# Optimization experiments

Measured on AMD Instinct MI355X. Metric: run time of the kernel, lower is better.

Reference implementation:

```python
import jax, jax.numpy as jnp
import numpy as np

INPUT_SIZE = 500
SENTENCE_SIZE = 128


def setup_inputs() -> dict:
    key = jax.random.key(0)
    ks = jax.random.split(key, 20)
    B, D = 16, 512
    Ho, Hi, Hu = 4, 4, 4
    dh_ori = D // Ho          # 128
    dh = D // (Hi + Hu)       # 64
    s = 0.05
    code = jax.random.normal(ks[0], (B, INPUT_SIZE, D), jnp.float32)
    # binary sentence-membership mask (which code tokens belong to each sentence)
    input_sentence = (jax.random.uniform(ks[1], (B, SENTENCE_SIZE, INPUT_SIZE)) < 0.2).astype(jnp.float32)

    def W(k, h, dout):
        return jax.random.normal(k, (h, D, dout), jnp.float32) * s

    def b(k, h, dout):
        return jax.random.normal(k, (h, dout), jnp.float32) * 0.01

    return dict(
        code=code, input_sentence=input_sentence,
        Wq_ori=W(ks[2], Ho, dh_ori), bq_ori=b(ks[3], Ho, dh_ori),
        Wk_ori=W(ks[4], Ho, dh_ori), bk_ori=b(ks[5], Ho, dh_ori),
        Wq_in=W(ks[6], Hi, dh), bq_in=b(ks[7], Hi, dh),
        Wk_in=W(ks[8], Hi, dh), bk_in=b(ks[9], Hi, dh),
        Wv_in=W(ks[10], Hi, dh), bv_in=b(ks[11], Hi, dh),
        Wq_out=W(ks[12], Hu, dh), bq_out=b(ks[13], Hu, dh),
        Wk_out=W(ks[14], Hu, dh), bk_out=b(ks[15], Hu, dh),
        Wv_out=W(ks[16], Hu, dh), bv_out=b(ks[17], Hu, dh),
    )


def _proj(x, W, b):
    # x: (B, N, D), W: (H, D, F), b: (H, F) -> (B, H, N, F), relu Dense per head
    return jax.nn.relu(jnp.einsum('bnd,hdf->bhnf', x, W) + b[:, None, :])


def reference(code, input_sentence,
              Wq_ori, bq_ori, Wk_ori, bk_ori,
              Wq_in, bq_in, Wk_in, bk_in, Wv_in, bv_in,
              Wq_out, bq_out, Wk_out, bk_out, Wv_out, bv_out):
    B, S = input_sentence.shape[0], input_sentence.shape[1]
    sent = input_sentence

    # ---- original (ori) branch: max over heads of raw QK^T, mask, matmul code ----
    q = _proj(code, Wq_ori, bq_ori)
    k = _proj(code, Wk_ori, bk_ori)
    scores_ori = jnp.einsum('bhnf,bhmf->bhnm', q, k).max(axis=1)      # (B, N, N)
    sA = jnp.einsum('bsn,bnm->bsm', sent, scores_ori)                 # (B, S, N)
    out_ori = jnp.einsum('bsm,bmd->bsd', sent * sA, code)             # (B, S, D)

    # ---- in-mask heads ----
    qi = _proj(code, Wq_in, bq_in)
    ki = _proj(code, Wk_in, bk_in)
    vi = _proj(code, Wv_in, bv_in)
    sc = jnp.einsum('bhnf,bhmf->bhnm', qi, ki)                        # (B, Hi, N, N)
    sAi = jnp.einsum('bsn,bhnm->bhsm', sent, sc)                      # (B, Hi, S, N)
    out_in = jnp.einsum('bhsm,bhmf->bhsf', sent[:, None] * sAi, vi)   # (B, Hi, S, F)

    # ---- out-mask heads ----
    qo = _proj(code, Wq_out, bq_out)
    ko = _proj(code, Wk_out, bk_out)
    vo = _proj(code, Wv_out, bv_out)
    sco = jnp.einsum('bhnf,bhmf->bhnm', qo, ko)
    sAo = jnp.einsum('bsn,bhnm->bhsm', sent, sco)
    masked = (sent - 1.0)[:, None] * sAo                              # (B, Hu, S, N)
    include = sent.sum(axis=2)[:, None, :, None]                      # (B, 1, S, 1)
    masked = masked / (INPUT_SIZE - include) * include
    out_out = jnp.einsum('bhsm,bhmf->bhsf', masked, vo)               # (B, Hu, S, F)

    # original returns a list [ori, in_0..in_Hi-1, out_0..out_Hu-1]; concat along features
    in_flat = jnp.transpose(out_in, (0, 2, 1, 3)).reshape(B, S, -1)
    out_flat = jnp.transpose(out_out, (0, 2, 1, 3)).reshape(B, S, -1)
    return jnp.concatenate([out_ori, in_flat, out_flat], axis=-1)
```

## Files before the change

kernel.cpp:

```cpp
#include <hip/hip_runtime.h>
#include <cfloat>

#define B_  16
#define N_  500
#define NP  512
#define S_  128
#define D_  512
#define FO  128
#define FI  64

typedef unsigned short u16;
typedef __attribute__((ext_vector_type(8))) short bf8;
typedef __attribute__((ext_vector_type(4))) float f4;

#define MFMA(a,b,c) __builtin_amdgcn_mfma_f32_16x16x32_bf16((a),(b),(c),0,0,0)

__device__ __forceinline__ u16 f2b(float x){
    union{float f;unsigned u;} v; v.f=x;
    unsigned r = v.u + 0x7fffu + ((v.u>>16)&1u);
    return (u16)(r>>16);
}
__device__ __forceinline__ float b2f(u16 x){
    union{unsigned u;float f;} v; v.u=((unsigned)x)<<16; return v.f;
}
__device__ __forceinline__ bf8 ldb8(const u16* p){ return *(const bf8*)p; }

__device__ __forceinline__ void gl2lds16(const u16* g, u16* lds){
    __builtin_amdgcn_global_load_lds(
        (const __attribute__((address_space(1))) unsigned int*)g,
        (__attribute__((address_space(3))) unsigned int*)lds, 16, 0, 0);
}

__global__ __launch_bounds__(256) void prep_code(const float* __restrict__ code,
                                                 u16* __restrict__ codeB,
                                                 u16* __restrict__ codeT)
{
    __shared__ float T[64][65];
    const int b = blockIdx.x, m0 = blockIdx.y*64, d0 = blockIdx.z*64;
    const int t = threadIdx.x;
    #pragma unroll
    for (int i=0;i<16;++i){
        int idx = t + i*256; int rr = idx>>6, cc = idx&63;
        int m = m0+rr;
        T[rr][cc] = (m < N_) ? code[((size_t)b*N_+m)*D_ + d0+cc] : 0.f;
    }
    __syncthreads();
    #pragma unroll
    for (int i=0;i<16;++i){
        int idx=t+i*256; int rr=idx>>6, cc=idx&63; int m=m0+rr;
        if (m<N_) codeB[((size_t)b*N_+m)*D_ + d0+cc] = f2b(T[rr][cc]);
    }
    #pragma unroll
    for (int i=0;i<16;++i){
        int idx=t+i*256; int dd=idx>>6, mm=idx&63;
        codeT[((size_t)b*D_ + d0+dd)*NP + m0+mm] = f2b(T[mm][dd]);
    }
}

__global__ __launch_bounds__(128) void prep_sent(const float* __restrict__ sent,
                                                 u16* __restrict__ sentB,
                                                 float* __restrict__ inc)
{
    const int b=blockIdx.x, s=blockIdx.y, t=threadIdx.x;
    const float* row = sent + ((size_t)b*S_+s)*N_;
    float4 v = make_float4(0.f,0.f,0.f,0.f);
    const int n = t*4;
    if (n < N_) v = *(const float4*)(row+n);
    float sum = v.x+v.y+v.z+v.w;
    ushort4 o; o.x=f2b(v.x); o.y=f2b(v.y); o.z=f2b(v.z); o.w=f2b(v.w);
    *(ushort4*)&sentB[((size_t)b*S_+s)*NP + n] = o;
    #pragma unroll
    for (int off=32; off; off>>=1) sum += __shfl_down(sum, off);
    __shared__ float ls[2];
    if ((t&63)==0) ls[t>>6]=sum;
    __syncthreads();
    if (t==0) inc[b*S_+s] = ls[0]+ls[1];
}

struct PWAll { const float* W[8]; u16* WT[8]; };
__global__ __launch_bounds__(256) void prep_w_all(PWAll a)
{
    const int slot = blockIdx.y;
    const int widx = slot<4 ? (slot>>1) : slot-2;
    const int ftile= slot<4 ? (slot&1)  : 0;
    const int F    = slot<4 ? 128 : 64;
    const float* W = a.W[widx];
    u16* WT        = a.WT[widx];
    __shared__ float T[64][65];
    const int h=blockIdx.x, f0=ftile*64, d0=blockIdx.z*64, t=threadIdx.x;
    #pragma unroll
    for (int i=0;i<16;++i){
        int idx=t+i*256; int rr=idx>>6, cc=idx&63;
        T[rr][cc] = W[((size_t)h*D_ + d0+rr)*F + f0+cc];
    }
    __syncthreads();
    #pragma unroll
    for (int i=0;i<16;++i){
        int idx=t+i*256; int ff=idx>>6, dd=idx&63;
        WT[((size_t)h*F + f0+ff)*D_ + d0+dd] = f2b(T[dd][ff]);
    }
}

__global__ __launch_bounds__(256) void zero_pad4(u16* a0, u16* a1, u16* a2, u16* a3)
{
    u16* arr4[4] = {a0,a1,a2,a3};
    u16* base = arr4[blockIdx.y] + (size_t)blockIdx.x*FI*NP;
    for (int idx=threadIdx.x; idx<FI*12; idx+=256){
        int f = idx/12, n = N_ + idx%12;
        base[(size_t)f*NP + n] = 0;
    }
}

struct GemmOut { const float* bias[8]; u16* dst[8]; };
__global__ __launch_bounds__(256) void proj_gemm(const u16* __restrict__ codeB,
                                                 const u16* __restrict__ WallT,
                                                 GemmOut go)
{
    __shared__ alignas(16) u16 As[2][128*32];
    __shared__ alignas(16) u16 Bs[2][128*32];
    const int t = threadIdx.x;
    const int w = t>>6, l = t&63, lane16 = l&15, lq = l>>4;
    const int r0 = blockIdx.x*128;
    const int c0 = blockIdx.y*128;
    const int wr = (w>>1)*64, wc = (w&1)*64;
    const int srow = l>>2;
    const int scol = (l&3)*8;

    f4 acc[4][4] = {};

    auto STAGE = [&](int buf, int k0){
        #pragma unroll
        for (int iss=0; iss<2; ++iss){
            const int rbase = w*32 + iss*16;
            gl2lds16(codeB + (size_t)(r0+rbase+srow)*D_ + k0 + scol, &As[buf][rbase*32]);
            gl2lds16(WallT + (size_t)(c0+rbase+srow)*D_ + k0 + scol, &Bs[buf][rbase*32]);
        }
    };

    STAGE(0, 0);
    int buf = 0;
    for (int k0=0; k0<D_; k0+=32){
        __syncthreads();
        if (k0+32 < D_) STAGE(buf^1, k0+32);
        bf8 af[4], bfr[4];
        #pragma unroll
        for (int i=0;i<4;++i){
            af[i]  = *(const bf8*)&As[buf][(wr + i*16 + lane16)*32 + lq*8];
            bfr[i] = *(const bf8*)&Bs[buf][(wc + i*16 + lane16)*32 + lq*8];
        }
        #pragma unroll
        for (int i=0;i<4;++i)
            #pragma unroll
            for (int j=0;j<4;++j)
                acc[i][j] = MFMA(af[i], bfr[j], acc[i][j]);
        buf ^= 1;
    }
    #pragma unroll
    for (int j=0;j<4;++j){
        const int c = c0 + wc + j*16 + lane16;
        int ri, hf, F;
        if (c < 1024){ ri = c>>9; hf = c & 511; F = 128; }
        else { const int u = c-1024; ri = 2 + (u>>8); hf = u & 255; F = 64; }
        const float bv = go.bias[ri][hf];
        const int h  = (F==128) ? (hf>>7) : (hf>>6);
        const int f2 = hf & (F-1);
        const bool tr = (ri>=2) && (ri!=3) && (ri!=6);
        #pragma unroll
        for (int i=0;i<4;++i){
            const int rb = r0 + wr + i*16 + lq*4;
            if (rb >= 8000) continue;
            const int b  = rb / 500;
            const int n0 = rb % 500;
            float v[4];
            #pragma unroll
            for (int reg=0;reg<4;++reg){
                float x = acc[i][j][reg] + bv;
                v[reg] = x>0.f ? x : 0.f;
            }
            if (tr){
                ushort4 o4; o4.x=f2b(v[0]); o4.y=f2b(v[1]); o4.z=f2b(v[2]); o4.w=f2b(v[3]);
                *(ushort4*)&go.dst[ri][((size_t)(b*4+h)*FI + f2)*NP + n0] = o4;
            } else {
                u16* o = go.dst[ri] + ((size_t)(b*4+h)*N_ + n0)*F + f2;
                #pragma unroll
                for (int reg=0;reg<4;++reg) o[(size_t)reg*F] = f2b(v[reg]);
            }
        }
    }
}

__global__ __launch_bounds__(256) void ms_mfma(const u16* __restrict__ q,
                                               const u16* __restrict__ k,
                                               u16* __restrict__ maxscT)
{
    __shared__ alignas(16) u16 Qs[64][136];
    __shared__ alignas(16) u16 Ks[128][136];
    const int t=threadIdx.x, w=t>>6, l=t&63, lane16=l&15, lq=l>>4;
    const int b=blockIdx.x, n0=blockIdx.y*64, m0=blockIdx.z*128;
    const int wr=(w>>1)*32, wc=(w&1)*64;

    f4 best[2][4];
    #pragma unroll
    for(int rt=0;rt<2;++rt)
        #pragma unroll
        for(int ct=0;ct<4;++ct)
            #pragma unroll
            for(int i=0;i<4;++i) best[rt][ct][i] = -FLT_MAX;

    for (int h=0;h<4;++h){
        const u16* qh = q + (size_t)(b*4+h)*N_*FO;
        const u16* kh = k + (size_t)(b*4+h)*N_*FO;
        #pragma unroll
        for (int i=0;i<4;++i){
            const int e=t+i*256, row=e>>4, kc=(e&15)*8;
            int n=n0+row; if(n>N_-1)n=N_-1;
            *(bf8*)&Qs[row][kc] = ldb8(qh + (size_t)n*FO + kc);
        }
        #pragma unroll
        for (int i=0;i<8;++i){
            const int e=t+i*256, row=e>>4, kc=(e&15)*8;
            int m=m0+row; if(m>N_-1)m=N_-1;
            *(bf8*)&Ks[row][kc] = ldb8(kh + (size_t)m*FO + kc);
        }
        __syncthreads();
        f4 acc[2][4]={};
        #pragma unroll
        for (int kk=0;kk<FO;kk+=32){
            bf8 a0=*(const bf8*)&Qs[wr+lane16][kk+lq*8];
            bf8 a1=*(const bf8*)&Qs[wr+16+lane16][kk+lq*8];
            #pragma unroll
            for(int ct=0;ct<4;++ct){
                bf8 bb=*(const bf8*)&Ks[wc+ct*16+lane16][kk+lq*8];
                acc[0][ct]=MFMA(a0,bb,acc[0][ct]);
                acc[1][ct]=MFMA(a1,bb,acc[1][ct]);
            }
        }
        #pragma unroll
        for(int rt=0;rt<2;++rt)
            #pragma unroll
            for(int ct=0;ct<4;++ct)
                #pragma unroll
                for(int i=0;i<4;++i) best[rt][ct][i] = fmaxf(best[rt][ct][i], acc[rt][ct][i]);
        __syncthreads();
    }
    #pragma unroll
    for(int rt=0;rt<2;++rt)
        #pragma unroll
        for(int ct=0;ct<4;++ct){
            const int m  = m0+wc+ct*16+lane16;
            const int nb = n0+wr+rt*16+lq*4;
            if (m < N_ && nb < N_){
                ushort4 o; o.x=f2b(best[rt][ct][0]); o.y=f2b(best[rt][ct][1]);
                o.z=f2b(best[rt][ct][2]); o.w=f2b(best[rt][ct][3]);
                *(ushort4*)&maxscT[((size_t)b*NP+m)*NP + nb] = o;
            }
        }
}

__global__ __launch_bounds__(512) void saoo(const u16* __restrict__ sentB,
                                            const u16* __restrict__ maxscT,
                                            const u16* __restrict__ codeT,
                                            float* __restrict__ out)
{
    __shared__ u16 sAmS[16][520];
    const int b=blockIdx.x, s0=blockIdx.y*16;
    const int t=threadIdx.x, w=t>>6, l=t&63, lane16=l&15, lq=l>>4;

    {
        const int m0 = w*64;
        const u16* ap = sentB + ((size_t)b*S_ + s0+lane16)*NP + lq*8;
        const u16* bp[4];
        #pragma unroll
        for(int ct=0;ct<4;++ct) bp[ct] = maxscT + ((size_t)b*NP + m0+ct*16+lane16)*NP + lq*8;
        f4 acc[4] = {};
        for (int k0=0;k0<NP;k0+=32){
            bf8 av=ldb8(ap+k0);
            #pragma unroll
            for(int ct=0;ct<4;++ct) acc[ct]=MFMA(av, ldb8(bp[ct]+k0), acc[ct]);
        }
        #pragma unroll
        for(int ct=0;ct<4;++ct){
            const int m = m0+ct*16+lane16;
            #pragma unroll
            for(int reg=0;reg<4;++reg){
                const int s = s0+lq*4+reg;
                const float sv = b2f(sentB[((size_t)b*S_+s)*NP+m]);
                sAmS[lq*4+reg][m] = f2b(acc[ct][reg]*sv);
            }
        }
    }
    __syncthreads();
    {
        const int d0 = w*64;
        const u16* bp[4];
        #pragma unroll
        for(int ct=0;ct<4;++ct) bp[ct] = codeT + ((size_t)b*D_ + d0+ct*16+lane16)*NP + lq*8;
        f4 acc[4] = {};
        for (int k0=0;k0<NP;k0+=32){
            bf8 av = *(const bf8*)&sAmS[lane16][k0+lq*8];
            #pragma unroll
            for(int ct=0;ct<4;++ct) acc[ct]=MFMA(av, ldb8(bp[ct]+k0), acc[ct]);
        }
        #pragma unroll
        for(int ct=0;ct<4;++ct){
            const int d = d0+ct*16+lane16;
            #pragma unroll
            for(int reg=0;reg<4;++reg){
                const int s = s0+lq*4+reg;
                out[((size_t)b*S_+s)*1024 + d] = acc[ct][reg];
            }
        }
    }
}

struct AttnArgs { const u16* qT[2]; const u16* kp[2]; const u16* vT[2]; };
__global__ __launch_bounds__(256) void attn_fused(AttnArgs a,
                                                  const u16* __restrict__ sentB,
                                                  const float* __restrict__ inc,
                                                  float* __restrict__ out)
{
    __shared__ float red[4][32][68];
    __shared__ u16 qsS[32][72];
    __shared__ u16 Pw[4][32][72];
    const int bh=blockIdx.x, b=bh>>2, h=bh&3, s0=blockIdx.y*32, br=blockIdx.z;
    const u16* qT = a.qT[br];
    const u16* kp = a.kp[br];
    const u16* vT = a.vT[br];
    const int t=threadIdx.x, w=t>>6, l=t&63, lane16=l&15, lq=l>>4;

    {
        const u16 *ap[2], *bp[4];
        #pragma unroll
        for(int rt=0;rt<2;++rt) ap[rt] = sentB + ((size_t)b*S_ + s0+rt*16+lane16)*NP + w*128 + lq*8;
        #pragma unroll
        for(int ct=0;ct<4;++ct) bp[ct] = qT + ((size_t)bh*FI + ct*16+lane16)*NP + w*128 + lq*8;
        f4 acc[2][4] = {};
        #pragma unroll
        for (int k0=0;k0<128;k0+=32){
            bf8 a0=ldb8(ap[0]+k0), a1=ldb8(ap[1]+k0);
            #pragma unroll
            for(int ct=0;ct<4;++ct){
                bf8 bb=ldb8(bp[ct]+k0);
                acc[0][ct]=MFMA(a0,bb,acc[0][ct]);
                acc[1][ct]=MFMA(a1,bb,acc[1][ct]);
            }
        }
        #pragma unroll
        for(int rt=0;rt<2;++rt)
            #pragma unroll
            for(int ct=0;ct<4;++ct)
                #pragma unroll
                for(int reg=0;reg<4;++reg)
                    red[w][rt*16+lq*4+reg][ct*16+lane16] = acc[rt][ct][reg];
    }
    __syncthreads();
    {
        const int s=t>>3, f0=(t&7)*8;
        #pragma unroll
        for (int j=0;j<8;++j){
            float v = red[0][s][f0+j]+red[1][s][f0+j]+red[2][s][f0+j]+red[3][s][f0+j];
            qsS[s][f0+j] = f2b(v);
        }
    }
    __syncthreads();

    f4 accO[2][4] = {};
    #pragma unroll
    for (int c=0;c<2;++c){
        const int m0 = w*64 + c*256;
        f4 p[2][4] = {};
        const u16* bp[4];
        #pragma unroll
        for(int ct=0;ct<4;++ct){
            int m=m0+ct*16+lane16; if(m>N_-1)m=N_-1;
            bp[ct] = kp + ((size_t)bh*N_+m)*FI + lq*8;
        }
        #pragma unroll
        for (int kk=0; kk<FI; kk+=32){
            bf8 a0 = *(const bf8*)&qsS[lane16][kk+lq*8];
            bf8 a1 = *(const bf8*)&qsS[16+lane16][kk+lq*8];
            #pragma unroll
            for(int ct=0;ct<4;++ct){
                bf8 bb=ldb8(bp[ct]+kk);
                p[0][ct]=MFMA(a0,bb,p[0][ct]);
                p[1][ct]=MFMA(a1,bb,p[1][ct]);
            }
        }
        #pragma unroll
        for(int rt=0;rt<2;++rt)
            #pragma unroll
            for(int ct=0;ct<4;++ct){
                const int m = m0+ct*16+lane16;
                #pragma unroll
                for(int reg=0;reg<4;++reg){
                    const int s = s0+rt*16+lq*4+reg;
                    const float sv = b2f(sentB[((size_t)b*S_+s)*NP+m]);
                    const float wgt = br ? ((m<N_)? sv-1.f : 0.f) : sv;
                    Pw[w][rt*16+lq*4+reg][ct*16+lane16] = f2b(p[rt][ct][reg]*wgt);
                }
            }
        #pragma unroll
        for (int kk2=0; kk2<64; kk2+=32){
            bf8 a2[2];
            #pragma unroll
            for(int rt=0;rt<2;++rt) a2[rt] = *(const bf8*)&Pw[w][rt*16+lane16][kk2+lq*8];
            #pragma unroll
            for(int ct=0;ct<4;++ct){
                bf8 vv = ldb8(vT + ((size_t)bh*FI + ct*16+lane16)*NP + m0+kk2+lq*8);
                accO[0][ct]=MFMA(a2[0],vv,accO[0][ct]);
                accO[1][ct]=MFMA(a2[1],vv,accO[1][ct]);
            }
        }
    }
    #pragma unroll
    for(int rt=0;rt<2;++rt)
        #pragma unroll
        for(int ct=0;ct<4;++ct)
            #pragma unroll
            for(int reg=0;reg<4;++reg)
                red[w][rt*16+lq*4+reg][ct*16+lane16] = accO[rt][ct][reg];
    __syncthreads();
    {
        const int s=t>>3, f0=(t&7)*8;
        float fac = 1.f;
        if (br){ const float ic = inc[b*S_+s0+s]; fac = ic/(500.f-ic); }
        const size_t o = ((size_t)b*S_+s0+s)*1024 + (br?768:512) + h*FI + f0;
        #pragma unroll
        for (int j=0;j<8;++j){
            float v = red[0][s][f0+j]+red[1][s][f0+j]+red[2][s][f0+j]+red[3][s][f0+j];
            out[o+j] = v*fac;
        }
    }
}

extern "C" void kernel_launch(void* const* d_in, const int* in_sizes, int n_in,
                              void* d_out, int out_size, void* d_ws, size_t ws_size,
                              hipStream_t stream)
{
    const float* code   = (const float*)d_in[0];
    const float* sent   = (const float*)d_in[1];
    const float* Wq_ori = (const float*)d_in[2];
    const float* bq_ori = (const float*)d_in[3];
    const float* Wk_ori = (const float*)d_in[4];
    const float* bk_ori = (const float*)d_in[5];
    const float* Wq_in  = (const float*)d_in[6];
    const float* bq_in  = (const float*)d_in[7];
    const float* Wk_in  = (const float*)d_in[8];
    const float* bk_in  = (const float*)d_in[9];
    const float* Wv_in  = (const float*)d_in[10];
    const float* bv_in  = (const float*)d_in[11];
    const float* Wq_out = (const float*)d_in[12];
    const float* bq_out = (const float*)d_in[13];
    const float* Wk_out = (const float*)d_in[14];
    const float* bk_out = (const float*)d_in[15];
    const float* Wv_out = (const float*)d_in[16];
    const float* bv_out = (const float*)d_in[17];
    float* out = (float*)d_out;

    char* w = (char*)d_ws;
    u16*   codeB  = (u16*)(w);
    u16*   WallT  = (u16*)(w + 8257536);
    u16*   WTqo   = WallT;
    u16*   WTko   = WallT +  262144;
    u16*   WTqi   = WallT +  524288;
    u16*   WTki   = WallT +  655360;
    u16*   WTvi   = WallT +  786432;
    u16*   WTqu   = WallT +  917504;
    u16*   WTku   = WallT + 1048576;
    u16*   WTvu   = WallT + 1179648;
    u16*   sentB  = (u16*)(w + 10878976);
    float* incp   = (float*)(w + 12976128);
    u16* q_ori  = (u16*)(w + 12984320);
    u16* k_ori  = (u16*)(w + 21176320);
    u16* maxscT = (u16*)(w + 29368320);
    u16* codeT  = (u16*)(w + 37756928);
    u16* k_in   = (u16*)(w + 46145536);
    u16* k_out  = (u16*)(w + 50241536);
    u16* qT_in  = (u16*)(w + 54337536);
    u16* qT_out = (u16*)(w + 58531840);
    u16* vT_in  = (u16*)(w + 62726144);
    u16* vT_out = (u16*)(w + 66920448);

    prep_code<<<dim3(16,8,8), 256, 0, stream>>>(code, codeB, codeT);
    prep_sent<<<dim3(16,128), 128, 0, stream>>>(sent, sentB, incp);
    PWAll pw;
    pw.W[0]=Wq_ori; pw.W[1]=Wk_ori; pw.W[2]=Wq_in; pw.W[3]=Wk_in;
    pw.W[4]=Wv_in;  pw.W[5]=Wq_out; pw.W[6]=Wk_out; pw.W[7]=Wv_out;
    pw.WT[0]=WTqo; pw.WT[1]=WTko; pw.WT[2]=WTqi; pw.WT[3]=WTki;
    pw.WT[4]=WTvi; pw.WT[5]=WTqu; pw.WT[6]=WTku; pw.WT[7]=WTvu;
    prep_w_all<<<dim3(4,10,8), 256, 0, stream>>>(pw);
    zero_pad4<<<dim3(64,4), 256, 0, stream>>>(qT_in, qT_out, vT_in, vT_out);

    GemmOut go;
    go.bias[0]=bq_ori; go.bias[1]=bk_ori; go.bias[2]=bq_in; go.bias[3]=bk_in;
    go.bias[4]=bv_in;  go.bias[5]=bq_out; go.bias[6]=bk_out; go.bias[7]=bv_out;
    go.dst[0]=q_ori; go.dst[1]=k_ori; go.dst[2]=qT_in; go.dst[3]=k_in;
    go.dst[4]=vT_in; go.dst[5]=qT_out; go.dst[6]=k_out; go.dst[7]=vT_out;
    proj_gemm<<<dim3(63,20), 256, 0, stream>>>(codeB, WallT, go);

    ms_mfma<<<dim3(16,8,4), 256, 0, stream>>>(q_ori, k_ori, maxscT);
    saoo<<<dim3(16,8), 512, 0, stream>>>(sentB, maxscT, codeT, out);

    AttnArgs aa;
    aa.qT[0]=qT_in;  aa.qT[1]=qT_out;
    aa.kp[0]=k_in;   aa.kp[1]=k_out;
    aa.vT[0]=vT_in;  aa.vT[1]=vT_out;
    attn_fused<<<dim3(64,4,2), 256, 0, stream>>>(aa, sentB, incp, out);
}
```

Baseline: 136.9 us.

## Stage proj_gemm epilogue through LDS for coalesced stores and remap blocks per XCD

The projection GEMM epilogue now writes biased, ReLU'd bf16 tiles into a shared-memory buffer that aliases the operand staging area, then streams them out as coalesced ushort4 rows in either the transposed or the natural layout. The launch changes to a 1D grid of 1280 blocks with an XCD-aware mapping, so blocks sharing row tiles of codeB land on the same XCD for L2 reuse. The K loop is unrolled by two with explicit vmcnt drains, and the workspace grows so 64 row tiles (8192 rows) of codeB fit. Smaller edits remove bounds checks in ms_mfma stores and skip the multiply when the sentence mask is zero. These add an extra LDS round trip and barrier, and the unguarded ms_mfma stores rely on padding being writable.

```diff
diff --git a/kernel.cpp b/kernel.cpp
--- a/kernel.cpp
+++ b/kernel.cpp
@@ -29,6 +29,9 @@
     __builtin_amdgcn_global_load_lds(
         (const __attribute__((address_space(1))) unsigned int*)g,
         (__attribute__((address_space(3))) unsigned int*)lds, 16, 0, 0);
+}
+__device__ __forceinline__ void vdrain(){
+    asm volatile("s_waitcnt vmcnt(0)" ::: "memory");
 }
 
 __global__ __launch_bounds__(256) void prep_code(const float* __restrict__ code,
@@ -112,79 +115,126 @@
 }
 
 struct GemmOut { const float* bias[8]; u16* dst[8]; };
+union ProjLDS {
+    u16 ab[4][4096];
+    u16 ot[16896];
+};
 __global__ __launch_bounds__(256) void proj_gemm(const u16* __restrict__ codeB,
                                                  const u16* __restrict__ WallT,
                                                  GemmOut go)
 {
-    __shared__ alignas(16) u16 As[2][128*32];
-    __shared__ alignas(16) u16 Bs[2][128*32];
+    __shared__ alignas(16) ProjLDS L;
+
     const int t = threadIdx.x;
     const int w = t>>6, l = t&63, lane16 = l&15, lq = l>>4;
-    const int r0 = blockIdx.x*128;
-    const int c0 = blockIdx.y*128;
+    const int bid = blockIdx.x;
+    const int xcd = bid & 7;
+    const int g   = bid >> 3;
+    const int rt  = xcd*8 + g/20;
+    const int ct  = g - (g/20)*20;
+    const int r0 = rt*128;
+    const int c0 = ct*128;
     const int wr = (w>>1)*64, wc = (w&1)*64;
     const int srow = l>>2;
     const int scol = (l&3)*8;
 
     f4 acc[4][4] = {};
 
-    auto STAGE = [&](int buf, int k0){
+    auto STAGE = [&](u16* Ad, u16* Bd, int k0){
         #pragma unroll
         for (int iss=0; iss<2; ++iss){
             const int rbase = w*32 + iss*16;
-            gl2lds16(codeB + (size_t)(r0+rbase+srow)*D_ + k0 + scol, &As[buf][rbase*32]);
-            gl2lds16(WallT + (size_t)(c0+rbase+srow)*D_ + k0 + scol, &Bs[buf][rbase*32]);
+            gl2lds16(codeB + (size_t)(r0+rbase+srow)*D_ + k0 + scol, Ad + rbase*32);
+            gl2lds16(WallT + (size_t)(c0+rbase+srow)*D_ + k0 + scol, Bd + rbase*32);
         }
     };
-
-    STAGE(0, 0);
-    int buf = 0;
-    for (int k0=0; k0<D_; k0+=32){
-        __syncthreads();
-        if (k0+32 < D_) STAGE(buf^1, k0+32);
+    auto COMPUTE = [&](const u16* Ad, const u16* Bd){
         bf8 af[4], bfr[4];
         #pragma unroll
         for (int i=0;i<4;++i){
-            af[i]  = *(const bf8*)&As[buf][(wr + i*16 + lane16)*32 + lq*8];
-            bfr[i] = *(const bf8*)&Bs[buf][(wc + i*16 + lane16)*32 + lq*8];
+            af[i]  = *(const bf8*)&Ad[(wr + i*16 + lane16)*32 + lq*8];
+            bfr[i] = *(const bf8*)&Bd[(wc + i*16 + lane16)*32 + lq*8];
         }
         #pragma unroll
         for (int i=0;i<4;++i)
             #pragma unroll
             for (int j=0;j<4;++j)
                 acc[i][j] = MFMA(af[i], bfr[j], acc[i][j]);
-        buf ^= 1;
-    }
+    };
+
+    STAGE(L.ab[0], L.ab[2], 0);
+    #pragma unroll
+    for (int k0=0; k0<D_; k0+=64){
+        vdrain(); __syncthreads();
+        if (k0+32 < D_) STAGE(L.ab[1], L.ab[3], k0+32);
+        COMPUTE(L.ab[0], L.ab[2]);
+        vdrain(); __syncthreads();
+        if (k0+64 < D_) STAGE(L.ab[0], L.ab[2], k0+64);
+        COMPUTE(L.ab[1], L.ab[3]);
+    }
+
+    const int ri = (ct<4) ? 0 : (ct<8) ? 1 : 2 + ((ct-8)>>1);
+    const bool tr = (ri==2)||(ri==4)||(ri==5)||(ri==7);
+
+    vdrain(); __syncthreads();
+
     #pragma unroll
     for (int j=0;j<4;++j){
         const int c = c0 + wc + j*16 + lane16;
-        int ri, hf, F;
-        if (c < 1024){ ri = c>>9; hf = c & 511; F = 128; }
-        else { const int u = c-1024; ri = 2 + (u>>8); hf = u & 255; F = 64; }
-        const float bv = go.bias[ri][hf];
-        const int h  = (F==128) ? (hf>>7) : (hf>>6);
-        const int f2 = hf & (F-1);
-        const bool tr = (ri>=2) && (ri!=3) && (ri!=6);
-        #pragma unroll
-        for (int i=0;i<4;++i){
-            const int rb = r0 + wr + i*16 + lq*4;
-            if (rb >= 8000) continue;
-            const int b  = rb / 500;
-            const int n0 = rb % 500;
-            float v[4];
-            #pragma unroll
-            for (int reg=0;reg<4;++reg){
-                float x = acc[i][j][reg] + bv;
-                v[reg] = x>0.f ? x : 0.f;
-            }
-            if (tr){
-                ushort4 o4; o4.x=f2b(v[0]); o4.y=f2b(v[1]); o4.z=f2b(v[2]); o4.w=f2b(v[3]);
-                *(ushort4*)&go.dst[ri][((size_t)(b*4+h)*FI + f2)*NP + n0] = o4;
-            } else {
-                u16* o = go.dst[ri] + ((size_t)(b*4+h)*N_ + n0)*F + f2;
+        const int idx = (c < 1024) ? (c & 511) : ((c-1024) & 255);
+        const float bv = go.bias[ri][idx];
+        if (tr){
+            #pragma unroll
+            for (int i=0;i<4;++i){
+                ushort4 o4;
+                float x0=acc[i][j][0]+bv, x1=acc[i][j][1]+bv, x2=acc[i][j][2]+bv, x3=acc[i][j][3]+bv;
+                o4.x=f2b(x0>0.f?x0:0.f); o4.y=f2b(x1>0.f?x1:0.f);
+                o4.z=f2b(x2>0.f?x2:0.f); o4.w=f2b(x3>0.f?x3:0.f);
+                *(ushort4*)&L.ot[(wc+j*16+lane16)*132 + wr+i*16+lq*4] = o4;
+            }
+        } else {
+            #pragma unroll
+            for (int i=0;i<4;++i)
                 #pragma unroll
-                for (int reg=0;reg<4;++reg) o[(size_t)reg*F] = f2b(v[reg]);
-            }
+                for (int reg=0;reg<4;++reg){
+                    float x = acc[i][j][reg] + bv;
+                    L.ot[(wr+i*16+lq*4+reg)*132 + wc+j*16+lane16] = f2b(x>0.f?x:0.f);
+                }
+        }
+    }
+    __syncthreads();
+
+    if (tr){
+        const int c  = t>>1;
+        const int cg = c0 + c;
+        const int u  = cg - 1024;
+        const int hfv = u & 255, h = hfv>>6, f2 = hfv & 63;
+        u16* dbase = go.dst[ri];
+        const int half = t & 1;
+        #pragma unroll
+        for (int k2=0;k2<16;++k2){
+            const int r  = half*64 + k2*4;
+            const int rb = r0 + r;
+            if (rb < 8000){
+                const int b = rb/500, n = rb - b*500;
+                *(ushort4*)&dbase[((size_t)(b*4+h)*FI + f2)*NP + n] =
+                    *(const ushort4*)&L.ot[c*132 + r];
+            }
+        }
+    } else {
+        const int r  = t>>1;
+        const int rb = r0 + r;
+        if (rb < 8000){
+            const int b = rb/500, n = rb - b*500;
+            const int half = t & 1;
+            const int cg0 = c0 + half*64;
+            int h, f2base, F2;
+            if (cg0 < 1024){ const int hf0 = cg0 & 511; h = hf0>>7; f2base = hf0 & 127; F2 = 128; }
+            else           { const int hf0 = (cg0-1024) & 255; h = hf0>>6; f2base = hf0 & 63; F2 = 64; }
+            u16* dstp = go.dst[ri] + ((size_t)(b*4+h)*N_ + n)*F2 + f2base;
+            #pragma unroll
+            for (int k2=0;k2<16;++k2)
+                *(ushort4*)&dstp[k2*4] = *(const ushort4*)&L.ot[r*132 + half*64 + k2*4];
         }
     }
 }
@@ -249,11 +299,9 @@
         for(int ct=0;ct<4;++ct){
             const int m  = m0+wc+ct*16+lane16;
             const int nb = n0+wr+rt*16+lq*4;
-            if (m < N_ && nb < N_){
-                ushort4 o; o.x=f2b(best[rt][ct][0]); o.y=f2b(best[rt][ct][1]);
-                o.z=f2b(best[rt][ct][2]); o.w=f2b(best[rt][ct][3]);
-                *(ushort4*)&maxscT[((size_t)b*NP+m)*NP + nb] = o;
-            }
+            ushort4 o; o.x=f2b(best[rt][ct][0]); o.y=f2b(best[rt][ct][1]);
+            o.z=f2b(best[rt][ct][2]); o.w=f2b(best[rt][ct][3]);
+            *(ushort4*)&maxscT[((size_t)b*NP+m)*NP + nb] = o;
         }
 }
 
@@ -285,7 +333,7 @@
             for(int reg=0;reg<4;++reg){
                 const int s = s0+lq*4+reg;
                 const float sv = b2f(sentB[((size_t)b*S_+s)*NP+m]);
-                sAmS[lq*4+reg][m] = f2b(acc[ct][reg]*sv);
+                sAmS[lq*4+reg][m] = (sv != 0.f) ? f2b(acc[ct][reg]*sv) : (u16)0;
             }
         }
     }
@@ -459,7 +507,7 @@
 
     char* w = (char*)d_ws;
     u16*   codeB  = (u16*)(w);
-    u16*   WallT  = (u16*)(w + 8257536);
+    u16*   WallT  = (u16*)(w + 8388608);
     u16*   WTqo   = WallT;
     u16*   WTko   = WallT +  262144;
     u16*   WTqi   = WallT +  524288;
@@ -468,18 +516,18 @@
     u16*   WTqu   = WallT +  917504;
     u16*   WTku   = WallT + 1048576;
     u16*   WTvu   = WallT + 1179648;
-    u16*   sentB  = (u16*)(w + 10878976);
-    float* incp   = (float*)(w + 12976128);
-    u16* q_ori  = (u16*)(w + 12984320);
-    u16* k_ori  = (u16*)(w + 21176320);
-    u16* maxscT = (u16*)(w + 29368320);
-    u16* codeT  = (u16*)(w + 37756928);
-    u16* k_in   = (u16*)(w + 46145536);
-    u16* k_out  = (u16*)(w + 50241536);
-    u16* qT_in  = (u16*)(w + 54337536);
-    u16* qT_out = (u16*)(w + 58531840);
-    u16* vT_in  = (u16*)(w + 62726144);
-    u16* vT_out = (u16*)(w + 66920448);
+    u16*   sentB  = (u16*)(w + 11010048);
+    float* incp   = (float*)(w + 13107200);
+    u16* q_ori  = (u16*)(w + 13115392);
+    u16* k_ori  = (u16*)(w + 21307392);
+    u16* maxscT = (u16*)(w + 29499392);
+    u16* codeT  = (u16*)(w + 37888000);
+    u16* k_in   = (u16*)(w + 46276608);
+    u16* k_out  = (u16*)(w + 50372608);
+    u16* qT_in  = (u16*)(w + 54468608);
+    u16* qT_out = (u16*)(w + 58662912);
+    u16* vT_in  = (u16*)(w + 62857216);
+    u16* vT_out = (u16*)(w + 67051520);
 
     prep_code<<<dim3(16,8,8), 256, 0, stream>>>(code, codeB, codeT);
     prep_sent<<<dim3(16,128), 128, 0, stream>>>(sent, sentB, incp);
@@ -496,7 +544,7 @@
     go.bias[4]=bv_in;  go.bias[5]=bq_out; go.bias[6]=bk_out; go.bias[7]=bv_out;
     go.dst[0]=q_ori; go.dst[1]=k_ori; go.dst[2]=qT_in; go.dst[3]=k_in;
     go.dst[4]=vT_in; go.dst[5]=qT_out; go.dst[6]=k_out; go.dst[7]=vT_out;
-    proj_gemm<<<dim3(63,20), 256, 0, stream>>>(codeB, WallT, go);
+    proj_gemm<<<dim3(1280), 256, 0, stream>>>(codeB, WallT, go);
 
     ms_mfma<<<dim3(16,8,4), 256, 0, stream>>>(q_ori, k_ori, maxscT);
     saoo<<<dim3(16,8), 512, 0, stream>>>(sentB, maxscT, codeT, out);
```

New measurement: 139.5 us. About the same (+1.9%).
